# Kernel optimization log

Hardware: AMD Instinct MI355X
Metric: run time of the kernel (lower is better)

## Reference

```python
import jax, jax.numpy as jnp
import numpy as np

DIM = 192
HEADS = 12
HEAD_DIM = DIM // HEADS  # 16
WS = (2, 2, 2)
MLP_HIDDEN = int(2.0 * DIM)
D = H = W = 32
LN_EPS = 1e-5


def setup_inputs() -> dict:
    key = jax.random.key(0)
    ks = jax.random.split(key, 8)
    s = 0.02

    def nrm(k, shape):
        return jax.random.normal(k, shape, jnp.float32) * s

    return {
        "x": jax.random.normal(ks[0], (1, D, H, W, DIM), jnp.float32),
        "xa": jax.random.normal(ks[1], (1, D, H, W, DIM), jnp.float32),
        "norm1_g": jnp.ones((DIM,), jnp.float32),
        "norm1_b": jnp.zeros((DIM,), jnp.float32),
        "norm2_g": jnp.ones((DIM,), jnp.float32),
        "norm2_b": jnp.zeros((DIM,), jnp.float32),
        "Wq": nrm(ks[2], (DIM, DIM)),
        "bq": jnp.zeros((DIM,), jnp.float32),
        "Wkv": nrm(ks[3], (DIM, 2 * DIM)),
        "bkv": jnp.zeros((2 * DIM,), jnp.float32),
        "Wp": nrm(ks[4], (DIM, DIM)),
        "bp": jnp.zeros((DIM,), jnp.float32),
        "W1": nrm(ks[5], (DIM, MLP_HIDDEN)),
        "b1": jnp.zeros((MLP_HIDDEN,), jnp.float32),
        "W2": nrm(ks[6], (MLP_HIDDEN, DIM)),
        "b2": jnp.zeros((DIM,), jnp.float32),
    }


def _ln(x, g, b):
    m = x.mean(-1, keepdims=True)
    v = ((x - m) ** 2).mean(-1, keepdims=True)
    return (x - m) * jax.lax.rsqrt(v + LN_EPS) * g + b


def _window_partition(x):
    # x: (D,H,W,C) -> (nW, N, C), N = prod(WS)
    d, h, w = D // WS[0], H // WS[1], W // WS[2]
    C = x.shape[-1]
    g = x.reshape(d, WS[0], h, WS[1], w, WS[2], C)
    g = g.transpose(0, 2, 4, 1, 3, 5, 6)  # (d,h,w,ws0,ws1,ws2,C)
    return g.reshape(d * h * w, WS[0] * WS[1] * WS[2], C)


def _window_area_partition(x):
    # 3x3x3 neighbor-window expansion with zero padding. Replicates the
    # source bug: neighbor slot 20 (offset (2,0,2)) is left as zeros.
    d, h, w = D // WS[0], H // WS[1], W // WS[2]
    C = x.shape[-1]
    g = x.reshape(d, WS[0], h, WS[1], w, WS[2], C)
    g = g.transpose(0, 2, 4, 1, 3, 5, 6)  # (d,h,w,ws0,ws1,ws2,C)
    p = jnp.pad(g, ((1, 1), (1, 1), (1, 1), (0, 0), (0, 0), (0, 0), (0, 0)))
    slabs = []
    for i in range(27):
        di, dj, dk = i // 9, (i // 3) % 3, i % 3
        if i == 20:
            slabs.append(jnp.zeros_like(g))
        else:
            slabs.append(p[di:di + d, dj:dj + h, dk:dk + w])
    b = jnp.stack(slabs, axis=3)  # (d,h,w,27,ws0,ws1,ws2,C)
    nW = d * h * w
    b = b.reshape(nW, 3, 3, 3, WS[0], WS[1], WS[2], C)
    b = b.transpose(0, 1, 4, 2, 5, 3, 6, 7)  # interleave neighbor/within axes
    return b.reshape(nW, 27 * WS[0] * WS[1] * WS[2], C)


def _window_reverse(win, C):
    # (nW,N,C) -> (D,H,W,C)
    d, h, w = D // WS[0], H // WS[1], W // WS[2]
    x = win.reshape(d, h, w, WS[0], WS[1], WS[2], C)
    x = x.transpose(0, 3, 1, 4, 2, 5, 6)
    return x.reshape(D, H, W, C)


def reference(x, xa, norm1_g, norm1_b, norm2_g, norm2_b,
              Wq, bq, Wkv, bkv, Wp, bp, W1, b1, W2, b2):
    C = DIM
    shortcut = x
    xn = _ln(x[0], norm1_g, norm1_b)
    xan = _ln(xa[0], norm1_g, norm1_b)

    x_win = _window_partition(xn)          # (nW, N, C)
    xa_win = _window_area_partition(xan)   # (nW, 27N, C)
    nW, N, _ = x_win.shape
    M = xa_win.shape[1]

    q = (x_win @ Wq + bq).reshape(nW, N, HEADS, HEAD_DIM)
    kv = (xa_win @ Wkv + bkv).reshape(nW, M, 2, HEADS, HEAD_DIM)
    k, v = kv[:, :, 0], kv[:, :, 1]

    scale = HEAD_DIM ** -0.5
    attn = jnp.einsum('bnhd,bmhd->bhnm', q * scale, k)
    attn = jax.nn.softmax(attn, axis=-1)
    out = jnp.einsum('bhnm,bmhd->bnhd', attn, v).reshape(nW, N, C)
    out = out @ Wp + bp

    x_attn = _window_reverse(out, C)[None]  # (1,D,H,W,C)
    x1 = shortcut + x_attn
    h_mlp = jax.nn.gelu(_ln(x1, norm2_g, norm2_b) @ W1 + b1, approximate=False)
    return x1 + (h_mlp @ W2 + b2)
```

## Files before the change

kernel.cpp:

```cpp
#include <hip/hip_runtime.h>
#include <hip/hip_bf16.h>
#include <math.h>


#define TOK 32768
#define NWIN 4096

typedef float f32x4 __attribute__((ext_vector_type(4)));
typedef float f32x16 __attribute__((ext_vector_type(16)));
typedef short bf16x8 __attribute__((ext_vector_type(8)));
typedef short bf16x4 __attribute__((ext_vector_type(4)));

static __device__ __forceinline__ short f2bf(float x) {
  __hip_bfloat16 h = __float2bfloat16(x);
  return __builtin_bit_cast(short, h);
}

enum { EP_RESID_LN = 2, EP_GELU = 3, EP_RESID = 4 };

static __device__ __forceinline__ void pack_one(const float* __restrict__ W,
                                                short* __restrict__ dst,
                                                int K, int N, int blk, int lane) {
  int KS = K / 32;
  int ks = blk % KS, c = blk / KS;
  int col = c * 16 + (lane & 15);
  int krow = ks * 32 + (lane >> 4) * 8;
  bf16x8 v;
#pragma unroll
  for (int j = 0; j < 8; ++j) v[j] = f2bf(W[(size_t)(krow + j) * N + col]);
  *(bf16x8*)(dst + ((size_t)blk * 64 + lane) * 8) = v;
}

__global__ __launch_bounds__(256) void prep_kernel(
    const float* __restrict__ Wq, const float* __restrict__ Wkv,
    const float* __restrict__ Wp, const float* __restrict__ W1,
    const float* __restrict__ W2, const float* __restrict__ bkv,
    short* __restrict__ wq_p, short* __restrict__ wkv_p, short* __restrict__ wp_p,
    short* __restrict__ w1_p, short* __restrict__ w2_p,
    short* __restrict__ kext, short* __restrict__ vext,
    int* __restrict__ gIdx) {
  int bid = blockIdx.x;
  int tid = threadIdx.x;
  if (bid < 144) {
    int pb = bid * 4 + (tid >> 6);
    int lane = tid & 63;
    if (pb < 72)        pack_one(Wq,  wq_p,  192, 192, pb,       lane);
    else if (pb < 216)  pack_one(Wkv, wkv_p, 192, 384, pb - 72,  lane);
    else if (pb < 288)  pack_one(Wp,  wp_p,  192, 192, pb - 216, lane);
    else if (pb < 432)  pack_one(W1,  w1_p,  192, 384, pb - 288, lane);
    else                pack_one(W2,  w2_p,  384, 192, pb - 432, lane);
  } else if (bid < 144 + NWIN) {
    int w = bid - 144;
    int m = tid;
    if (m >= 224) return;
    int ww = w & 15, wh = (w >> 4) & 15, wd = w >> 8;
    int t = TOK;
    if (m < 216) {
      int lw = m & 1;  int t1 = m >> 1;
      int dk = t1 % 3; int t2 = t1 / 3;
      int lh = t2 & 1; int t3 = t2 >> 1;
      int dj = t3 % 3; int t4 = t3 / 3;
      int ld = t4 & 1; int di = t4 >> 1;
      int nwd = wd + di - 1, nwh = wh + dj - 1, nww = ww + dk - 1;
      int slab = di * 9 + dj * 3 + dk;
      if (nwd >= 0 && nwd <= 15 && nwh >= 0 && nwh <= 15 && nww >= 0 && nww <= 15 && slab != 20) {
        t = ((nwd * 2 + ld) * 32 + (nwh * 2 + lh)) * 32 + (nww * 2 + lw);
      }
    }
    gIdx[w * 224 + m] = t * 384;
  } else {
    if (tid < 192)      kext[tid] = f2bf(bkv[tid]);
    else if (tid < 384) vext[tid - 192] = f2bf(bkv[tid]);
  }
}

__global__ __launch_bounds__(256, 2) void qkv_gemm(
    const float* __restrict__ x, const float* __restrict__ xa,
    const short* __restrict__ wq_p, const short* __restrict__ wkv_p,
    const float* __restrict__ bq, const float* __restrict__ bkv,
    const float* __restrict__ lg, const float* __restrict__ lb,
    short* __restrict__ qb, short* __restrict__ kb, short* __restrict__ vb) {
  __shared__ __align__(16) short Bls[72 * 512];
  const int y = blockIdx.y;
  const int lane = threadIdx.x & 63;
  const int wv = threadIdx.x >> 6;
  const int lrow = lane & 15, lkg = lane >> 4;
  const int rb = blockIdx.x * 64 + wv * 16;

  const float* Av = (y == 0) ? x : xa;
  const short* Bp = (y == 0) ? wq_p : wkv_p + (size_t)(y - 1) * 72 * 512;

  {
#pragma unroll
    for (int i = 0; i < 18; ++i) {
      int ch = wv * 18 + i;
      __builtin_amdgcn_global_load_lds(
          (const __attribute__((address_space(1))) void*)(Bp + (size_t)ch * 512 + lane * 8),
          (__attribute__((address_space(3))) void*)(Bls + ch * 512), 16, 0, 0);
    }
  }

  bf16x8 af[6];
  {
    const float* Arow = Av + (size_t)(rb + lrow) * 192 + lkg * 8;
    float v[6][8];
    float s = 0.f;
#pragma unroll
    for (int ks = 0; ks < 6; ++ks) {
      float4 lo = *(const float4*)(Arow + ks * 32);
      float4 hi = *(const float4*)(Arow + ks * 32 + 4);
      v[ks][0] = lo.x; v[ks][1] = lo.y; v[ks][2] = lo.z; v[ks][3] = lo.w;
      v[ks][4] = hi.x; v[ks][5] = hi.y; v[ks][6] = hi.z; v[ks][7] = hi.w;
#pragma unroll
      for (int j = 0; j < 8; ++j) s += v[ks][j];
    }
    s += __shfl_xor(s, 16); s += __shfl_xor(s, 32);
    float mean = s * (1.f / 192.f);
    float vs = 0.f;
#pragma unroll
    for (int ks = 0; ks < 6; ++ks)
#pragma unroll
      for (int j = 0; j < 8; ++j) { float d = v[ks][j] - mean; vs += d * d; }
    vs += __shfl_xor(vs, 16); vs += __shfl_xor(vs, 32);
    float rstd = rsqrtf(vs * (1.f / 192.f) + 1e-5f);
#pragma unroll
    for (int ks = 0; ks < 6; ++ks)
#pragma unroll
      for (int j = 0; j < 8; ++j) {
        int ch = ks * 32 + lkg * 8 + j;
        af[ks][j] = f2bf((v[ks][j] - mean) * rstd * lg[ch] + lb[ch]);
      }
  }
  __syncthreads();

  f32x4 acc[12];
#pragma unroll
  for (int c = 0; c < 12; ++c) acc[c] = (f32x4){0.f, 0.f, 0.f, 0.f};
#pragma unroll
  for (int ks = 0; ks < 6; ++ks)
#pragma unroll
    for (int c = 0; c < 12; ++c) {
      bf16x8 bfr = *(const bf16x8*)(Bls + ((c * 6 + ks) * 64 + lane) * 8);
      acc[c] = __builtin_amdgcn_mfma_f32_16x16x32_bf16(af[ks], bfr, acc[c], 0, 0, 0);
    }

  if (y == 0) {
#pragma unroll
    for (int c = 0; c < 12; ++c) {
      int col = c * 16 + lrow;
      float bia = bq[col];
#pragma unroll
      for (int i = 0; i < 4; ++i) {
        int row = rb + lkg * 4 + i;
        qb[(size_t)row * 192 + col] = f2bf((acc[c][i] + bia) * 0.36067376022224085f);
      }
    }
  } else {
    int nb = (y - 1) * 192;
#pragma unroll
    for (int c = 0; c < 12; ++c) {
      int col = nb + c * 16 + lrow;
      float bia = bkv[col];
#pragma unroll
      for (int i = 0; i < 4; ++i) {
        int row = rb + lkg * 4 + i;
        float v = acc[c][i] + bia;
        if (col < 192) kb[(size_t)row * 192 + col] = f2bf(v);
        else           vb[(size_t)row * 192 + col - 192] = f2bf(v);
      }
    }
  }
}

template <int EPI, int MT, int CT, int K, int NTOT>
__global__ __launch_bounds__(256, 2) void gemm_mfma(const void* __restrict__ Av,
                                                    const short* __restrict__ Bp,
                                                    const float* __restrict__ bias,
                                                    const float* __restrict__ resid,
                                                    const float* __restrict__ lg,
                                                    const float* __restrict__ lb,
                                                    void* __restrict__ C0v,
                                                    void* __restrict__ C1v) {
  constexpr int KS = K / 32;
  constexpr int CHUNKS = CT * KS;
  static_assert(CHUNKS == 72);
  __shared__ __align__(16) short Bls[CHUNKS * 512];

  const int lane = threadIdx.x & 63;
  const int wv = threadIdx.x >> 6;
  const int lrow = lane & 15, lkg = lane >> 4;
  const int rb = blockIdx.x * (64 * MT) + wv * (16 * MT);
  const int nb = blockIdx.y * (CT * 16);
  const int nb16 = blockIdx.y * CT;

  {
    const short* bsrc = Bp + (size_t)nb16 * KS * 512;
#pragma unroll
    for (int i = 0; i < 18; ++i) {
      int ch = wv * 18 + i;
      __builtin_amdgcn_global_load_lds(
          (const __attribute__((address_space(1))) void*)(bsrc + (size_t)ch * 512 + lane * 8),
          (__attribute__((address_space(3))) void*)(Bls + ch * 512), 16, 0, 0);
    }
  }

  bf16x8 af[MT][KS];
#pragma unroll
  for (int mt = 0; mt < MT; ++mt) {
    const short* Arow = (const short*)Av + (size_t)(rb + mt * 16 + lrow) * K + lkg * 8;
#pragma unroll
    for (int ks = 0; ks < KS; ++ks) af[mt][ks] = *(const bf16x8*)(Arow + ks * 32);
  }
  __syncthreads();

  f32x4 acc[MT][CT];
#pragma unroll
  for (int mt = 0; mt < MT; ++mt)
#pragma unroll
    for (int c = 0; c < CT; ++c) acc[mt][c] = (f32x4){0.f, 0.f, 0.f, 0.f};
#pragma unroll
  for (int ks = 0; ks < KS; ++ks) {
#pragma unroll
    for (int c = 0; c < CT; ++c) {
      bf16x8 bfr = *(const bf16x8*)(Bls + ((c * KS + ks) * 64 + lane) * 8);
#pragma unroll
      for (int mt = 0; mt < MT; ++mt)
        acc[mt][c] = __builtin_amdgcn_mfma_f32_16x16x32_bf16(af[mt][ks], bfr, acc[mt][c], 0, 0, 0);
    }
  }

  if constexpr (EPI == EP_RESID_LN) {
    static_assert(CT == 12);
#pragma unroll
    for (int mt = 0; mt < MT; ++mt) {
#pragma unroll
      for (int c = 0; c < 12; ++c) {
        int col = c * 16 + lrow;
        float bia = bias[col];
#pragma unroll
        for (int i = 0; i < 4; ++i) {
          int row = rb + mt * 16 + lkg * 4 + i;
          acc[mt][c][i] += bia + resid[(size_t)row * 192 + col];
          ((float*)C0v)[(size_t)row * 192 + col] = acc[mt][c][i];
        }
      }
#pragma unroll
      for (int i = 0; i < 4; ++i) {
        int row = rb + mt * 16 + lkg * 4 + i;
        float s2 = 0.f;
#pragma unroll
        for (int c = 0; c < 12; ++c) s2 += acc[mt][c][i];
        s2 += __shfl_xor(s2, 1); s2 += __shfl_xor(s2, 2);
        s2 += __shfl_xor(s2, 4); s2 += __shfl_xor(s2, 8);
        float mean = s2 * (1.f / 192.f);
        float vs2 = 0.f;
#pragma unroll
        for (int c = 0; c < 12; ++c) { float d = acc[mt][c][i] - mean; vs2 += d * d; }
        vs2 += __shfl_xor(vs2, 1); vs2 += __shfl_xor(vs2, 2);
        vs2 += __shfl_xor(vs2, 4); vs2 += __shfl_xor(vs2, 8);
        float rstd = rsqrtf(vs2 * (1.f / 192.f) + 1e-5f);
#pragma unroll
        for (int c = 0; c < 12; ++c) {
          int col = c * 16 + lrow;
          ((short*)C1v)[(size_t)row * 192 + col] =
              f2bf((acc[mt][c][i] - mean) * rstd * lg[col] + lb[col]);
        }
      }
    }
  } else {
#pragma unroll
    for (int mt = 0; mt < MT; ++mt)
#pragma unroll
      for (int c = 0; c < CT; ++c) {
        int col = nb + c * 16 + lrow;
        float bia = bias[col];
#pragma unroll
        for (int i = 0; i < 4; ++i) {
          int row = rb + mt * 16 + lkg * 4 + i;
          float v = acc[mt][c][i] + bia;
          if constexpr (EPI == EP_RESID) {
            ((float*)C0v)[(size_t)row * NTOT + col] = v + resid[(size_t)row * NTOT + col];
          } else {
            float gg = 0.5f * v * (1.f + erff(v * 0.70710678118654752f));
            ((short*)C0v)[(size_t)row * NTOT + col] = f2bf(gg);
          }
        }
      }
  }
}

__global__ __launch_bounds__(128, 3) void attn_mfma(const short* __restrict__ qbuf,
                                                    const short* __restrict__ kbuf,
                                                    const short* __restrict__ vbuf,
                                                    const int* __restrict__ gIdx,
                                                    short* __restrict__ obuf) {
  __shared__ __align__(16) short VsS[2][224 * 16];
  __shared__ __align__(16) short PsS[2][8 * 232];

  const int tid = threadIdx.x;
  const int wv = tid >> 6;
  const int lane = tid & 63;
  const int lrow = lane & 15, lkg = lane >> 4;
  const int l31 = lane & 31, kg2 = lane >> 5;

  unsigned bid = blockIdx.x;
  unsigned u = (bid & 7u) * 3072u + (bid >> 3);
  int w = (int)(u / 6u);
  int h = (int)(u % 6u) * 2 + wv;
  const int ww = w & 15, wh = (w >> 4) & 15, wd = w >> 8;
  const int wbase = wd * 2048 + wh * 64 + ww * 2;

  short* Vs = VsS[wv];
  short* Ps = PsS[wv];

  int* PsI = (int*)Ps;
  if (lane < 56) {
    int4 idx4 = ((const int4*)(gIdx + (size_t)w * 224))[lane];
    ((int4*)PsI)[lane] = idx4;
  }

  bf16x8 qa = (bf16x8)0;
  if (l31 < 8) {
    int n = l31;
    int tq = wbase + (n >> 2) * 1024 + ((n >> 1) & 1) * 32 + (n & 1);
    qa = *(const bf16x8*)(qbuf + (size_t)tq * 192 + h * 16 + kg2 * 8);
  }

  int ti7[7];
#pragma unroll
  for (int T = 0; T < 7; ++T) ti7[T] = PsI[T * 32 + l31];
  int mv7[7];
#pragma unroll
  for (int k = 0; k < 7; ++k) mv7[k] = PsI[(lane >> 1) + k * 32];

  const unsigned ko = (unsigned)(h * 32 + kg2 * 16);
  bf16x8 kf[7];
#pragma unroll
  for (int T = 0; T < 7; ++T)
    kf[T] = *(const bf16x8*)((const char*)kbuf + (unsigned)ti7[T] + ko);

  const unsigned vo = (unsigned)(h * 32 + (lane & 1) * 16);
  bf16x8 vv[7];
#pragma unroll
  for (int k = 0; k < 7; ++k)
    vv[k] = *(const bf16x8*)((const char*)vbuf + (unsigned)mv7[k] + vo);

  const f32x16 zero16 = (f32x16)0.f;
  float sum[4] = {0.f, 0.f, 0.f, 0.f};
#pragma unroll
  for (int T = 0; T < 7; ++T) {
    f32x16 c = __builtin_amdgcn_mfma_f32_32x32x16_bf16(qa, kf[T], zero16, 0, 0, 0);
#pragma unroll
    for (int r = 0; r < 4; ++r) {
      float sv = c[r];
      if (T == 6 && l31 >= 24) sv = -1e30f;
      float p = exp2f(sv);
      sum[r] += p;
      Ps[(r + 4 * kg2) * 232 + T * 32 + l31] = f2bf(p);
    }
  }

  float invq[4];
#pragma unroll
  for (int r = 0; r < 4; ++r) {
    float s = sum[r];
    s += __shfl_xor(s, 1);
    s += __shfl_xor(s, 2);
    s += __shfl_xor(s, 4);
    s += __shfl_xor(s, 8);
    s += __shfl_xor(s, 16);
    float iv = 1.f / s;
    float oth = __shfl_xor(iv, 32);
    invq[r] = (lane & 16) ? oth : iv;
  }

#pragma unroll
  for (int k = 0; k < 7; ++k)
    *(bf16x8*)(Vs + ((unsigned)lane + (unsigned)k * 64u) * 8u) = vv[k];
  asm volatile("s_waitcnt lgkmcnt(0)" ::: "memory");
  __builtin_amdgcn_sched_barrier(0);

  unsigned vbadr = (unsigned)(size_t)((__attribute__((address_space(3))) short*)Vs)
                 + (unsigned)(lkg * 256 + (lrow >> 2) * 32 + (lane & 3) * 8);
  bf16x4 t0[7], t1[7];
#pragma unroll
  for (int T = 0; T < 7; ++T) {
    unsigned a = vbadr + (unsigned)(T * 1024);
    asm volatile("ds_read_b64_tr_b16 %0, %1" : "=v"(t0[T]) : "v"(a));
    asm volatile("ds_read_b64_tr_b16 %0, %1 offset:128" : "=v"(t1[T]) : "v"(a));
  }
  bf16x8 pa[7];
#pragma unroll
  for (int T = 0; T < 7; ++T) {
    pa[T] = (bf16x8)0;
    if (lrow < 8) pa[T] = *(const bf16x8*)(Ps + lrow * 232 + T * 32 + lkg * 8);
  }
  asm volatile("s_waitcnt lgkmcnt(0)" ::: "memory");
  __builtin_amdgcn_sched_barrier(0);
  f32x4 o = {0.f, 0.f, 0.f, 0.f};
#pragma unroll
  for (int T = 0; T < 7; ++T) {
    bf16x8 vf = __builtin_shufflevector(t0[T], t1[T], 0, 1, 2, 3, 4, 5, 6, 7);
    o = __builtin_amdgcn_mfma_f32_16x16x32_bf16(pa[T], vf, o, 0, 0, 0);
  }

  if (lane < 32) {
#pragma unroll
    for (int r = 0; r < 4; ++r) {
      int n = (lane >> 4) * 4 + r;
      int tq = wbase + (n >> 2) * 1024 + ((n >> 1) & 1) * 32 + (n & 1);
      obuf[(size_t)tq * 192 + h * 16 + lrow] = f2bf(o[r] * invq[r]);
    }
  }
}

extern "C" void kernel_launch(void* const* d_in, const int* in_sizes, int n_in,
                              void* d_out, int out_size, void* d_ws, size_t ws_size,
                              hipStream_t stream) {
  const float* x   = (const float*)d_in[0];
  const float* xa  = (const float*)d_in[1];
  const float* n1g = (const float*)d_in[2];
  const float* n1b = (const float*)d_in[3];
  const float* n2g = (const float*)d_in[4];
  const float* n2b = (const float*)d_in[5];
  const float* Wq  = (const float*)d_in[6];
  const float* bq  = (const float*)d_in[7];
  const float* Wkv = (const float*)d_in[8];
  const float* bkv = (const float*)d_in[9];
  const float* Wp  = (const float*)d_in[10];
  const float* bp  = (const float*)d_in[11];
  const float* W1  = (const float*)d_in[12];
  const float* b1  = (const float*)d_in[13];
  const float* W2  = (const float*)d_in[14];
  const float* b2  = (const float*)d_in[15];

  char* wsb = (char*)d_ws;
  const size_t BB = (size_t)TOK * 192 * 2;
  short* attn_o = (short*)(wsb + 0 * BB);
  short* xn2    = (short*)(wsb + 1 * BB);
  short* qb     = (short*)(wsb + 2 * BB);
  short* kb     = (short*)(wsb + 3 * BB);
  short* vb     = (short*)(wsb + 4 * BB + 4096);
  float* x1     = (float*)(wsb + 5 * BB + 8192);
  char* p = wsb + 7 * BB + 16384;
  int* gIdx = (int*)p;            p += (size_t)NWIN * 224 * 4;
  short* wq_p  = (short*)p;       p += 192 * 192 * 2;
  short* wkv_p = (short*)p;       p += 192 * 384 * 2;
  short* wp_p  = (short*)p;       p += 192 * 192 * 2;
  short* w1_p  = (short*)p;       p += 192 * 384 * 2;
  short* w2_p  = (short*)p;       p += 384 * 192 * 2;

  short* hmlp = qb;

  prep_kernel<<<144 + NWIN + 1, 256, 0, stream>>>(
      Wq, Wkv, Wp, W1, W2, bkv, wq_p, wkv_p, wp_p, w1_p, w2_p,
      kb + (size_t)TOK * 192, vb + (size_t)TOK * 192, gIdx);

  qkv_gemm<<<dim3(512, 3), 256, 0, stream>>>(
      x, xa, wq_p, wkv_p, bq, bkv, n1g, n1b, qb, kb, vb);

  attn_mfma<<<NWIN * 6, 128, 0, stream>>>(qb, kb, vb, gIdx, attn_o);

  gemm_mfma<EP_RESID_LN, 2, 12, 192, 192><<<dim3(256, 1), 256, 0, stream>>>(
      attn_o, wp_p, bp, x, n2g, n2b, x1, xn2);

  gemm_mfma<EP_GELU, 2, 12, 192, 384><<<dim3(256, 2), 256, 0, stream>>>(
      xn2, w1_p, b1, nullptr, nullptr, nullptr, hmlp, nullptr);
  gemm_mfma<EP_RESID, 2, 6, 384, 192><<<dim3(256, 2), 256, 0, stream>>>(
      hmlp, w2_p, b2, x1, nullptr, nullptr, (float*)d_out, nullptr);
}
```

Before: 171.8 us.

## Process two heads per wave in attention kernel with prefetched K/V for second head

Each wave now handles two heads (hA and hB) instead of one, halving the grid to NWIN*3 blocks. The gather indices and Q loads are amortized across both heads, and the K/V gathers for the second head are issued before the first head's PV stage so their latency overlaps compute. This raises register pressure (two sets of K/V fragments live at once) under launch_bounds(128,3) and halves available parallelism.

```diff
diff --git a/kernel.cpp b/kernel.cpp
--- a/kernel.cpp
+++ b/kernel.cpp
@@ -304,9 +304,11 @@
   const int l31 = lane & 31, kg2 = lane >> 5;
 
   unsigned bid = blockIdx.x;
-  unsigned u = (bid & 7u) * 3072u + (bid >> 3);
-  int w = (int)(u / 6u);
-  int h = (int)(u % 6u) * 2 + wv;
+  unsigned u = (bid & 7u) * 1536u + (bid >> 3);
+  int w = (int)(u / 3u);
+  int qd = (int)(u % 3u);
+  const int hA = qd * 4 + wv;
+  const int hB = hA + 2;
   const int ww = w & 15, wh = (w >> 4) & 15, wd = w >> 8;
   const int wbase = wd * 2048 + wh * 64 + ww * 2;
 
@@ -318,98 +320,172 @@
     int4 idx4 = ((const int4*)(gIdx + (size_t)w * 224))[lane];
     ((int4*)PsI)[lane] = idx4;
   }
-
-  bf16x8 qa = (bf16x8)0;
+  int ti7[7];
+#pragma unroll
+  for (int T = 0; T < 7; ++T) ti7[T] = PsI[T * 32 + l31];
+  int mv7[7];
+#pragma unroll
+  for (int k = 0; k < 7; ++k) mv7[k] = PsI[(lane >> 1) + k * 32];
+
+  bf16x8 qaA = (bf16x8)0, qaB = (bf16x8)0;
   if (l31 < 8) {
     int n = l31;
     int tq = wbase + (n >> 2) * 1024 + ((n >> 1) & 1) * 32 + (n & 1);
-    qa = *(const bf16x8*)(qbuf + (size_t)tq * 192 + h * 16 + kg2 * 8);
-  }
-
-  int ti7[7];
-#pragma unroll
-  for (int T = 0; T < 7; ++T) ti7[T] = PsI[T * 32 + l31];
-  int mv7[7];
-#pragma unroll
-  for (int k = 0; k < 7; ++k) mv7[k] = PsI[(lane >> 1) + k * 32];
-
-  const unsigned ko = (unsigned)(h * 32 + kg2 * 16);
-  bf16x8 kf[7];
-#pragma unroll
-  for (int T = 0; T < 7; ++T)
-    kf[T] = *(const bf16x8*)((const char*)kbuf + (unsigned)ti7[T] + ko);
-
-  const unsigned vo = (unsigned)(h * 32 + (lane & 1) * 16);
-  bf16x8 vv[7];
-#pragma unroll
-  for (int k = 0; k < 7; ++k)
-    vv[k] = *(const bf16x8*)((const char*)vbuf + (unsigned)mv7[k] + vo);
-
+    const short* qp = qbuf + (size_t)tq * 192;
+    qaA = *(const bf16x8*)(qp + hA * 16 + kg2 * 8);
+    qaB = *(const bf16x8*)(qp + hB * 16 + kg2 * 8);
+  }
+
+  const unsigned lko = (unsigned)(kg2 * 16);
+  const unsigned lvo = (unsigned)((lane & 1) * 16);
+  unsigned vbadr = (unsigned)(size_t)((__attribute__((address_space(3))) short*)Vs)
+                 + (unsigned)(lkg * 256 + (lrow >> 2) * 32 + (lane & 3) * 8);
   const f32x16 zero16 = (f32x16)0.f;
-  float sum[4] = {0.f, 0.f, 0.f, 0.f};
+
+  bf16x8 kfA[7], vvA[7];
+  {
+    const unsigned ko = (unsigned)(hA * 32) + lko;
+    const unsigned vo = (unsigned)(hA * 32) + lvo;
+#pragma unroll
+    for (int T = 0; T < 7; ++T)
+      kfA[T] = *(const bf16x8*)((const char*)kbuf + (unsigned)ti7[T] + ko);
+#pragma unroll
+    for (int k = 0; k < 7; ++k)
+      vvA[k] = *(const bf16x8*)((const char*)vbuf + (unsigned)mv7[k] + vo);
+  }
+
+  float sumA[4] = {0.f, 0.f, 0.f, 0.f};
 #pragma unroll
   for (int T = 0; T < 7; ++T) {
-    f32x16 c = __builtin_amdgcn_mfma_f32_32x32x16_bf16(qa, kf[T], zero16, 0, 0, 0);
+    f32x16 c = __builtin_amdgcn_mfma_f32_32x32x16_bf16(qaA, kfA[T], zero16, 0, 0, 0);
 #pragma unroll
     for (int r = 0; r < 4; ++r) {
       float sv = c[r];
       if (T == 6 && l31 >= 24) sv = -1e30f;
       float p = exp2f(sv);
-      sum[r] += p;
+      sumA[r] += p;
       Ps[(r + 4 * kg2) * 232 + T * 32 + l31] = f2bf(p);
     }
   }
-
-  float invq[4];
+  float invqA[4];
 #pragma unroll
   for (int r = 0; r < 4; ++r) {
-    float s = sum[r];
-    s += __shfl_xor(s, 1);
-    s += __shfl_xor(s, 2);
-    s += __shfl_xor(s, 4);
-    s += __shfl_xor(s, 8);
-    s += __shfl_xor(s, 16);
+    float s = sumA[r];
+    s += __shfl_xor(s, 1); s += __shfl_xor(s, 2); s += __shfl_xor(s, 4);
+    s += __shfl_xor(s, 8); s += __shfl_xor(s, 16);
     float iv = 1.f / s;
     float oth = __shfl_xor(iv, 32);
-    invq[r] = (lane & 16) ? oth : iv;
-  }
-
-#pragma unroll
-  for (int k = 0; k < 7; ++k)
-    *(bf16x8*)(Vs + ((unsigned)lane + (unsigned)k * 64u) * 8u) = vv[k];
-  asm volatile("s_waitcnt lgkmcnt(0)" ::: "memory");
-  __builtin_amdgcn_sched_barrier(0);
-
-  unsigned vbadr = (unsigned)(size_t)((__attribute__((address_space(3))) short*)Vs)
-                 + (unsigned)(lkg * 256 + (lrow >> 2) * 32 + (lane & 3) * 8);
-  bf16x4 t0[7], t1[7];
+    invqA[r] = (lane & 16) ? oth : iv;
+  }
+
+  bf16x8 kfB[7], vvB[7];
+  {
+    const unsigned ko = (unsigned)(hB * 32) + lko;
+    const unsigned vo = (unsigned)(hB * 32) + lvo;
+#pragma unroll
+    for (int T = 0; T < 7; ++T)
+      kfB[T] = *(const bf16x8*)((const char*)kbuf + (unsigned)ti7[T] + ko);
+#pragma unroll
+    for (int k = 0; k < 7; ++k)
+      vvB[k] = *(const bf16x8*)((const char*)vbuf + (unsigned)mv7[k] + vo);
+  }
+
+  {
+#pragma unroll
+    for (int k = 0; k < 7; ++k)
+      *(bf16x8*)(Vs + ((unsigned)lane + (unsigned)k * 64u) * 8u) = vvA[k];
+    asm volatile("s_waitcnt lgkmcnt(0)" ::: "memory");
+    __builtin_amdgcn_sched_barrier(0);
+
+    bf16x4 t0[7], t1[7];
+#pragma unroll
+    for (int T = 0; T < 7; ++T) {
+      unsigned a = vbadr + (unsigned)(T * 1024);
+      asm volatile("ds_read_b64_tr_b16 %0, %1" : "=v"(t0[T]) : "v"(a));
+      asm volatile("ds_read_b64_tr_b16 %0, %1 offset:128" : "=v"(t1[T]) : "v"(a));
+    }
+    bf16x8 pa[7];
+#pragma unroll
+    for (int T = 0; T < 7; ++T) {
+      pa[T] = (bf16x8)0;
+      if (lrow < 8) pa[T] = *(const bf16x8*)(Ps + lrow * 232 + T * 32 + lkg * 8);
+    }
+    asm volatile("s_waitcnt lgkmcnt(0)" ::: "memory");
+    __builtin_amdgcn_sched_barrier(0);
+    f32x4 o = {0.f, 0.f, 0.f, 0.f};
+#pragma unroll
+    for (int T = 0; T < 7; ++T) {
+      bf16x8 vf = __builtin_shufflevector(t0[T], t1[T], 0, 1, 2, 3, 4, 5, 6, 7);
+      o = __builtin_amdgcn_mfma_f32_16x16x32_bf16(pa[T], vf, o, 0, 0, 0);
+    }
+    if (lane < 32) {
+#pragma unroll
+      for (int r = 0; r < 4; ++r) {
+        int n = (lane >> 4) * 4 + r;
+        int tq = wbase + (n >> 2) * 1024 + ((n >> 1) & 1) * 32 + (n & 1);
+        obuf[(size_t)tq * 192 + hA * 16 + lrow] = f2bf(o[r] * invqA[r]);
+      }
+    }
+  }
+
+  float sumB[4] = {0.f, 0.f, 0.f, 0.f};
 #pragma unroll
   for (int T = 0; T < 7; ++T) {
-    unsigned a = vbadr + (unsigned)(T * 1024);
-    asm volatile("ds_read_b64_tr_b16 %0, %1" : "=v"(t0[T]) : "v"(a));
-    asm volatile("ds_read_b64_tr_b16 %0, %1 offset:128" : "=v"(t1[T]) : "v"(a));
-  }
-  bf16x8 pa[7];
-#pragma unroll
-  for (int T = 0; T < 7; ++T) {
-    pa[T] = (bf16x8)0;
-    if (lrow < 8) pa[T] = *(const bf16x8*)(Ps + lrow * 232 + T * 32 + lkg * 8);
-  }
-  asm volatile("s_waitcnt lgkmcnt(0)" ::: "memory");
-  __builtin_amdgcn_sched_barrier(0);
-  f32x4 o = {0.f, 0.f, 0.f, 0.f};
-#pragma unroll
-  for (int T = 0; T < 7; ++T) {
-    bf16x8 vf = __builtin_shufflevector(t0[T], t1[T], 0, 1, 2, 3, 4, 5, 6, 7);
-    o = __builtin_amdgcn_mfma_f32_16x16x32_bf16(pa[T], vf, o, 0, 0, 0);
-  }
-
-  if (lane < 32) {
+    f32x16 c = __builtin_amdgcn_mfma_f32_32x32x16_bf16(qaB, kfB[T], zero16, 0, 0, 0);
 #pragma unroll
     for (int r = 0; r < 4; ++r) {
-      int n = (lane >> 4) * 4 + r;
-      int tq = wbase + (n >> 2) * 1024 + ((n >> 1) & 1) * 32 + (n & 1);
-      obuf[(size_t)tq * 192 + h * 16 + lrow] = f2bf(o[r] * invq[r]);
+      float sv = c[r];
+      if (T == 6 && l31 >= 24) sv = -1e30f;
+      float p = exp2f(sv);
+      sumB[r] += p;
+      Ps[(r + 4 * kg2) * 232 + T * 32 + l31] = f2bf(p);
+    }
+  }
+  float invqB[4];
+#pragma unroll
+  for (int r = 0; r < 4; ++r) {
+    float s = sumB[r];
+    s += __shfl_xor(s, 1); s += __shfl_xor(s, 2); s += __shfl_xor(s, 4);
+    s += __shfl_xor(s, 8); s += __shfl_xor(s, 16);
+    float iv = 1.f / s;
+    float oth = __shfl_xor(iv, 32);
+    invqB[r] = (lane & 16) ? oth : iv;
+  }
+  {
+#pragma unroll
+    for (int k = 0; k < 7; ++k)
+      *(bf16x8*)(Vs + ((unsigned)lane + (unsigned)k * 64u) * 8u) = vvB[k];
+    asm volatile("s_waitcnt lgkmcnt(0)" ::: "memory");
+    __builtin_amdgcn_sched_barrier(0);
+
+    bf16x4 t0[7], t1[7];
+#pragma unroll
+    for (int T = 0; T < 7; ++T) {
+      unsigned a = vbadr + (unsigned)(T * 1024);
+      asm volatile("ds_read_b64_tr_b16 %0, %1" : "=v"(t0[T]) : "v"(a));
+      asm volatile("ds_read_b64_tr_b16 %0, %1 offset:128" : "=v"(t1[T]) : "v"(a));
+    }
+    bf16x8 pa[7];
+#pragma unroll
+    for (int T = 0; T < 7; ++T) {
+      pa[T] = (bf16x8)0;
+      if (lrow < 8) pa[T] = *(const bf16x8*)(Ps + lrow * 232 + T * 32 + lkg * 8);
+    }
+    asm volatile("s_waitcnt lgkmcnt(0)" ::: "memory");
+    __builtin_amdgcn_sched_barrier(0);
+    f32x4 o = {0.f, 0.f, 0.f, 0.f};
+#pragma unroll
+    for (int T = 0; T < 7; ++T) {
+      bf16x8 vf = __builtin_shufflevector(t0[T], t1[T], 0, 1, 2, 3, 4, 5, 6, 7);
+      o = __builtin_amdgcn_mfma_f32_16x16x32_bf16(pa[T], vf, o, 0, 0, 0);
+    }
+    if (lane < 32) {
+#pragma unroll
+      for (int r = 0; r < 4; ++r) {
+        int n = (lane >> 4) * 4 + r;
+        int tq = wbase + (n >> 2) * 1024 + ((n >> 1) & 1) * 32 + (n & 1);
+        obuf[(size_t)tq * 192 + hB * 16 + lrow] = f2bf(o[r] * invqB[r]);
+      }
     }
   }
 }
@@ -459,7 +535,7 @@
   qkv_gemm<<<dim3(512, 3), 256, 0, stream>>>(
       x, xa, wq_p, wkv_p, bq, bkv, n1g, n1b, qb, kb, vb);
 
-  attn_mfma<<<NWIN * 6, 128, 0, stream>>>(qb, kb, vb, gIdx, attn_o);
+  attn_mfma<<<NWIN * 3, 128, 0, stream>>>(qb, kb, vb, gIdx, attn_o);
 
   gemm_mfma<EP_RESID_LN, 2, 12, 192, 192><<<dim3(256, 1), 256, 0, stream>>>(
       attn_o, wp_p, bp, x, n2g, n2b, x1, xn2);
```

Result: no change. 170.9 us (-0.6%).
